# Kernel optimization log

Hardware: AMD Instinct MI355X
Metric: run time of the kernel (lower is better)

Reference implementation:

```python
import jax, jax.numpy as jnp
import numpy as np

NUM_HEADS = 16

def _alibi(S, H, dtype):
    # fairseq-style ALiBi: slopes[h] * -(|i-j|), H assumed power of 2
    start = 2.0 ** (-8.0 / H)
    slopes = start ** jnp.arange(1, H + 1, dtype=jnp.float32)      # [H]
    pos = jnp.arange(S)
    rel = -jnp.abs(pos[None, :] - pos[:, None]).astype(jnp.float32)  # [S,S]
    return (slopes[:, None, None] * rel).astype(dtype)             # [H,S,S]

def setup_inputs() -> dict:
    key = jax.random.key(0)
    kx, km, kw1, kw2 = jax.random.split(key, 4)
    B, S, D = 2, 2048, 1024
    inputs = jax.random.normal(kx, (B, S, D), dtype=jnp.float32)
    mask = jax.random.bernoulli(km, 0.9, (B, S))
    mask = mask.at[:, 0].set(True)  # ensure each row has a valid key
    Wqkv = jax.random.normal(kw1, (3 * D, D), dtype=jnp.float32) * 0.02
    bqkv = jnp.zeros((3 * D,), dtype=jnp.float32)
    Wproj = jax.random.normal(kw2, (D, D), dtype=jnp.float32) * 0.02
    bproj = jnp.zeros((D,), dtype=jnp.float32)
    return {"inputs": inputs, "mask": mask, "Wqkv": Wqkv, "bqkv": bqkv,
            "Wproj": Wproj, "bproj": bproj}

def reference(inputs, mask, Wqkv, bqkv, Wproj, bproj):
    B, S, D = inputs.shape
    H = NUM_HEADS
    dh = D // H
    scale = D ** (-0.5)  # NOTE: original scales by full dim, not head dim
    qkv = inputs @ Wqkv.T + bqkv                       # [B,S,3D]
    qkv = qkv.reshape(B, S, H, 3 * dh).transpose(0, 2, 1, 3)  # [B,H,S,3dh]
    q, k, v = qkv[..., :dh], qkv[..., dh:2 * dh], qkv[..., 2 * dh:]
    attn = jnp.einsum('bhqd,bhkd->bhqk', q, k) * scale  # [B,H,S,S]
    attn = attn + _alibi(S, H, attn.dtype)[None]
    attn = jnp.where(mask[:, None, None, :], attn, jnp.finfo(attn.dtype).min)
    attn = jax.nn.softmax(attn, axis=-1)
    x = jnp.einsum('bhqk,bhkd->bhqd', attn, v)          # [B,H,S,dh]
    x = x.transpose(0, 2, 1, 3).reshape(B, S, D)
    return x @ Wproj.T + bproj
```

## Files before the change

### kernel.cpp

```cpp
#include <hip/hip_runtime.h>
#include <cstdint>
#include <cstddef>

#define B_  2
#define S_  2048
#define D_  1024
#define H_  16
#define DH_ 64
#define M_  (B_*S_)
#define N3_ (3*D_)
#define NT_ (S_/64)

typedef float f32x4 __attribute__((ext_vector_type(4)));
typedef short short8 __attribute__((ext_vector_type(8)));
typedef int   i32x4 __attribute__((ext_vector_type(4)));
typedef unsigned short u16x8 __attribute__((ext_vector_type(8)));
typedef unsigned short u16x4 __attribute__((ext_vector_type(4)));
typedef unsigned short u16x2 __attribute__((ext_vector_type(2)));

__device__ __forceinline__ unsigned short f2bf(float x) {
    unsigned int u = __float_as_uint(x);
    unsigned int r = (u + 0x7FFFu + ((u >> 16) & 1u)) >> 16;
    return (unsigned short)r;
}

__device__ __forceinline__ float exp2_(float x) { return __builtin_amdgcn_exp2f(x); }

__device__ __forceinline__ unsigned int cvt_pk_bf16(float a, float b) {
    unsigned int r;
    asm volatile("v_cvt_pk_bf16_f32 %0, %1, %2" : "=v"(r) : "v"(a), "v"(b));
    return r;
}

__device__ __forceinline__ int s3x(int row) {
    return (((row & 3) | (((row >> 3) & 1) << 2)) << 4);
}

__device__ __forceinline__ int xcd_swizzle(int lin, int nwg) {
    const int cpx = nwg >> 3;
    return (lin & 7) * cpx + (lin >> 3);
}

__device__ __forceinline__ void gload16(const void* g, void* l) {
    __builtin_amdgcn_global_load_lds(
        (const __attribute__((address_space(1))) unsigned int*)g,
        (__attribute__((address_space(3))) unsigned int*)l,
        16, 0, 0);
}

__global__ void k_mask(const unsigned char* __restrict__ mb, float* __restrict__ maskbias) {
    __shared__ int sBig, sM4, sM8;
    if (threadIdx.x == 0) { sBig = 0; sM4 = 0; sM8 = 0; }
    __syncthreads();
    int big = 0, m4 = 0, m8 = 0;
    for (int i = threadIdx.x; i < 4096; i += 256) {
        unsigned char v = mb[i];
        if (v > 1) big = 1;
        if (v && (i & 3)) m4 = 1;
        if (v && ((i & 7) == 4)) m8 = 1;
    }
    if (big) atomicOr(&sBig, 1);
    if (m4)  atomicOr(&sM4, 1);
    if (m8)  atomicOr(&sM8, 1);
    __syncthreads();
    const int w = sBig ? 0 : (sM4 ? 1 : (sM8 ? 4 : 8));
    const int i = blockIdx.x * 256 + threadIdx.x;
    bool on;
    if (w == 0)      on = ((const float*)mb)[i] != 0.0f;
    else if (w == 1) on = mb[i] != 0;
    else if (w == 4) on = ((const int*)mb)[i] != 0;
    else             on = ((const long long*)mb)[i] != 0;
    maskbias[i] = on ? 0.0f : -1e30f;
}

__global__ void k_f2bf3(const float* __restrict__ A, const float* __restrict__ B2,
                        const float* __restrict__ C, unsigned short* __restrict__ oA,
                        unsigned short* __restrict__ oB, unsigned short* __restrict__ oC) {
    const int nA = M_ * D_, nB = N3_ * D_, nC = D_ * D_;
    int i = (blockIdx.x * 256 + threadIdx.x) * 4;
    const float* src; unsigned short* dst; int off;
    if (i < nA)           { src = A;  dst = oA; off = i; }
    else if (i < nA + nB) { src = B2; dst = oB; off = i - nA; }
    else if (i < nA + nB + nC) { src = C; dst = oC; off = i - nA - nB; }
    else return;
    float4 v = *reinterpret_cast<const float4*>(&src[off]);
    u16x4 o = { f2bf(v.x), f2bf(v.y), f2bf(v.z), f2bf(v.w) };
    *reinterpret_cast<u16x4*>(&dst[off]) = o;
}

template <bool OUT_BF16>
__global__ __launch_bounds__(512) void k_gemm_bf16_cv(
    const unsigned short* __restrict__ A, const unsigned short* __restrict__ W,
    const float* __restrict__ bias, void* __restrict__ Cout,
    int M, int N, int K) {
    __shared__ __align__(16) unsigned short Al[3][128 * 64];
    __shared__ __align__(16) unsigned short Wl[3][128 * 64];

    const int tid  = threadIdx.x;
    const int lane = tid & 63;
    const int w    = tid >> 6;
    const int wr   = w >> 2, wc = w & 3;
    const int l16  = lane & 15, g = lane >> 4;
    const int m0 = blockIdx.y * 128, n0 = blockIdx.x * 128;
    const int NTk = K >> 6;

    f32x4 acc[4][2];
#pragma unroll
    for (int m = 0; m < 4; ++m)
#pragma unroll
        for (int n = 0; n < 2; ++n) acc[m][n] = (f32x4){0.f, 0.f, 0.f, 0.f};

    auto issueTile = [&](int kt) {
        const int k0 = kt << 6;
        unsigned short* Ad = Al[kt % 3];
        unsigned short* Wd = Wl[kt % 3];
#pragma unroll
        for (int i = 0; i < 2; ++i) {
            const int c = i * 512 + tid;
            const int row = c >> 3;
            const int colel = (((c & 7) ^ (row & 7)) << 3);
            gload16(A + (size_t)(m0 + row) * K + k0 + colel, Ad + c * 8);
            gload16(W + (size_t)(n0 + row) * K + k0 + colel, Wd + c * 8);
        }
    };

    issueTile(0);
    issueTile(1);

    for (int t = 0; t < NTk; ++t) {
        if (t + 2 < NTk) issueTile(t + 2);

        if (t < NTk - 2)       asm volatile("s_waitcnt vmcnt(8)" ::: "memory");
        else if (t == NTk - 2) asm volatile("s_waitcnt vmcnt(4)" ::: "memory");
        else                   asm volatile("s_waitcnt vmcnt(0)" ::: "memory");
        __builtin_amdgcn_s_barrier();
        __builtin_amdgcn_sched_barrier(0);

        const unsigned short* Ab = Al[t % 3];
        const unsigned short* Wb = Wl[t % 3];
        short8 a[4][2], b[2][2];
#pragma unroll
        for (int m = 0; m < 4; ++m)
#pragma unroll
            for (int kk = 0; kk < 2; ++kk) {
                const int row = wr * 64 + m * 16 + l16;
                const int kb = (kk * 64 + g * 16) ^ ((row & 7) << 4);
                a[m][kk] = *reinterpret_cast<const short8*>(
                    (const char*)Ab + row * 128 + kb);
            }
#pragma unroll
        for (int n = 0; n < 2; ++n)
#pragma unroll
            for (int kk = 0; kk < 2; ++kk) {
                const int row = wc * 32 + n * 16 + l16;
                const int kb = (kk * 64 + g * 16) ^ ((row & 7) << 4);
                b[n][kk] = *reinterpret_cast<const short8*>(
                    (const char*)Wb + row * 128 + kb);
            }

        __builtin_amdgcn_s_setprio(1);
#pragma unroll
        for (int kk = 0; kk < 2; ++kk)
#pragma unroll
            for (int m = 0; m < 4; ++m)
#pragma unroll
                for (int n = 0; n < 2; ++n)
                    acc[m][n] = __builtin_amdgcn_mfma_f32_16x16x32_bf16(
                        a[m][kk], b[n][kk], acc[m][n], 0, 0, 0);
        __builtin_amdgcn_s_setprio(0);

        __builtin_amdgcn_sched_barrier(0);
        __builtin_amdgcn_s_barrier();
    }

    float bv[2];
#pragma unroll
    for (int n = 0; n < 2; ++n) bv[n] = bias[n0 + wc * 32 + n * 16 + l16];
#pragma unroll
    for (int m = 0; m < 4; ++m) {
#pragma unroll
        for (int r = 0; r < 4; ++r) {
            const size_t row = m0 + wr * 64 + m * 16 + g * 4 + r;
#pragma unroll
            for (int n = 0; n < 2; ++n) {
                const int col = n0 + wc * 32 + n * 16 + l16;
                float v = acc[m][n][r] + bv[n];
                if (OUT_BF16)
                    ((unsigned short*)Cout)[row * N + col] = f2bf(v);
                else
                    ((float*)Cout)[row * N + col] = v;
            }
        }
    }
}

__global__ __launch_bounds__(512, 4) void k_attn_mfma(
    const unsigned short* __restrict__ qkv,
    const float* __restrict__ maskbias,
    unsigned short* __restrict__ x) {
    __shared__ __align__(16) unsigned short Kt[2][64][64];
    __shared__ __align__(16) unsigned short Vt[3][64][64];

    const int tid  = threadIdx.x;
    const int lane = tid & 63;
    const int wq   = tid >> 6;
    const int g    = lane >> 4;
    const int g4   = g * 4;
    const int l16  = lane & 15;

    const int nqt = S_ / 128;
    const int nwg = B_ * H_ * nqt;
    const int bid = xcd_swizzle(blockIdx.x, nwg);
    const int qt = bid % nqt;
    const int h  = (bid / nqt) % H_;
    const int b  = bid / (nqt * H_);
    const int q0 = qt * 128;
    const size_t rowbase = (size_t)b * S_ * N3_;
    const int hq = h * 192, hk = hq + 64, hv = hq + 128;
    const unsigned short* kvb = qkv + rowbase;
    const float* mbp = maskbias + b * S_;

    const int blrow = 8 * (l16 >> 2) + (l16 & 3);
    const int KBJ[4] = { 0, 4, 32, 36 };

    const unsigned short* qrp = kvb + (size_t)(q0 + wq * 16 + l16) * N3_ + hq;
    const short8 qa0 = *reinterpret_cast<const short8*>(qrp + g * 8);
    const short8 qa1 = *reinterpret_cast<const short8*>(qrp + 32 + g * 8);

    const int krow = tid >> 3;
    const int kgr  = tid & 7;
    const int vkb4 = (tid & 31) * 4;
    const int vdb  = (tid >> 5) * 4;
    u16x8 kr;
    u16x4 vr0, vr1;

    const int kwOff = (kgr << 4) ^ s3x(krow);

    {
        kr  = *reinterpret_cast<const u16x8*>(kvb + (size_t)krow * N3_ + hk + kgr * 8);
        const unsigned short* vs = kvb + (size_t)((tid & 31) * 2) * N3_ + hv + vdb;
        vr0 = *reinterpret_cast<const u16x4*>(vs);
        vr1 = *reinterpret_cast<const u16x4*>(vs + N3_);
        *reinterpret_cast<u16x8*>((char*)&Kt[0][krow][0] + kwOff) = kr;
#pragma unroll
        for (int j = 0; j < 4; ++j)
            *reinterpret_cast<u16x2*>((char*)&Vt[0][vdb + j][0] + (vkb4 ^ s3x(vdb + j))) =
                (u16x2){vr0[j], vr1[j]};
    }
    __syncthreads();

    f32x4 Oacc[4];
#pragma unroll
    for (int df = 0; df < 4; ++df) Oacc[df] = (f32x4){0.f, 0.f, 0.f, 0.f};
    float m = -1e30f, l = 0.0f;

    const float LOG2E = 1.4426950408889634f;
    const float c1 = 0.03125f * LOG2E;
    const float c2 = exp2f(-0.5f * (float)(h + 1)) * LOG2E;
    const int   qw0 = q0 + wq * 16;
    const int   qg  = qw0 + l16;
    const float alg = c2 * (float)(8 * g);
    float albr[4];
#pragma unroll
    for (int r = 0; r < 4; ++r) albr[r] = c2 * (float)r;
    const float ckb[4] = { 0.0f, c2 * 4.0f, c2 * 32.0f, c2 * 36.0f };

    const int sK = s3x(blrow);
    const int kr0Off = (g << 4) ^ sK;
    const int kr1Off = ((4 + g) << 4) ^ sK;
    const int sV = s3x(l16);
    const int vr0Off = (g << 4) ^ sV;
    const int vr1Off = ((4 + g) << 4) ^ sV;

    float p_[4][4];

    {
        kr  = *reinterpret_cast<const u16x8*>(kvb + (size_t)(64 + krow) * N3_ + hk + kgr * 8);
        const unsigned short* vs = kvb + (size_t)(64 + (tid & 31) * 2) * N3_ + hv + vdb;
        vr0 = *reinterpret_cast<const u16x4*>(vs);
        vr1 = *reinterpret_cast<const u16x4*>(vs + N3_);

        __builtin_amdgcn_s_setprio(1);
#pragma unroll
        for (int jb = 0; jb < 4; ++jb) {
            const char* rowp = (const char*)&Kt[0][blrow + KBJ[jb]][0];
            short8 kb0 = *reinterpret_cast<const short8*>(rowp + kr0Off);
            short8 kb1 = *reinterpret_cast<const short8*>(rowp + kr1Off);
            f32x4 c = (f32x4){0.f, 0.f, 0.f, 0.f};
            c = __builtin_amdgcn_mfma_f32_16x16x32_bf16(kb0, qa0, c, 0, 0, 0);
            c = __builtin_amdgcn_mfma_f32_16x16x32_bf16(kb1, qa1, c, 0, 0, 0);
#pragma unroll
            for (int r = 0; r < 4; ++r) p_[jb][r] = c[r];
        }
        __builtin_amdgcn_s_setprio(0);

        *reinterpret_cast<u16x8*>((char*)&Kt[1][krow][0] + kwOff) = kr;
#pragma unroll
        for (int j = 0; j < 4; ++j)
            *reinterpret_cast<u16x2*>((char*)&Vt[1][vdb + j][0] + (vkb4 ^ s3x(vdb + j))) =
                (u16x2){vr0[j], vr1[j]};
    }
    __syncthreads();
    {
        kr  = *reinterpret_cast<const u16x8*>(kvb + (size_t)(128 + krow) * N3_ + hk + kgr * 8);
        const unsigned short* vs = kvb + (size_t)(128 + (tid & 31) * 2) * N3_ + hv + vdb;
        vr0 = *reinterpret_cast<const u16x4*>(vs);
        vr1 = *reinterpret_cast<const u16x4*>(vs + N3_);
    }

    int vb_r = 0;
    int vb_w = 2;

    for (int t = 1; t < NT_ + 1; ++t) {
        const int k0m = (t - 1) * 64;

        f32x4 amv[4];
#pragma unroll
        for (int jb = 0; jb < 4; ++jb)
            amv[jb] = *reinterpret_cast<const f32x4*>(&mbp[k0m + 8 * g + KBJ[jb]]);

        f32x4 cnx[4];
        if (t < NT_) {
            const unsigned short (*Kc)[64] = Kt[t & 1];
            __builtin_amdgcn_s_setprio(1);
#pragma unroll
            for (int jb = 0; jb < 4; ++jb) {
                const char* rowp = (const char*)&Kc[blrow + KBJ[jb]][0];
                short8 kb0 = *reinterpret_cast<const short8*>(rowp + kr0Off);
                short8 kb1 = *reinterpret_cast<const short8*>(rowp + kr1Off);
                f32x4 c = (f32x4){0.f, 0.f, 0.f, 0.f};
                c = __builtin_amdgcn_mfma_f32_16x16x32_bf16(kb0, qa0, c, 0, 0, 0);
                c = __builtin_amdgcn_mfma_f32_16x16x32_bf16(kb1, qa1, c, 0, 0, 0);
                cnx[jb] = c;
            }
            __builtin_amdgcn_s_setprio(0);
        }

        if (k0m + 64 <= qw0) {
            const float tbg = c2 * (float)(k0m - qg) + alg;
#pragma unroll
            for (int jb = 0; jb < 4; ++jb) {
                const float tbj = tbg + ckb[jb];
#pragma unroll
                for (int r = 0; r < 4; ++r)
                    p_[jb][r] = fmaf(p_[jb][r], c1, tbj + albr[r] + amv[jb][r]);
            }
        } else if (k0m >= qw0 + 16) {
            const float tbg = c2 * (float)(k0m - qg) + alg;
#pragma unroll
            for (int jb = 0; jb < 4; ++jb) {
                const float tbj = -tbg - ckb[jb];
#pragma unroll
                for (int r = 0; r < 4; ++r)
                    p_[jb][r] = fmaf(p_[jb][r], c1, tbj - albr[r] + amv[jb][r]);
            }
        } else {
            const int dbase = k0m - qg + 8 * g;
#pragma unroll
            for (int jb = 0; jb < 4; ++jb)
#pragma unroll
                for (int r = 0; r < 4; ++r) {
                    int d = dbase + KBJ[jb] + r;
                    d = d < 0 ? -d : d;
                    p_[jb][r] = fmaf(p_[jb][r], c1, amv[jb][r] - c2 * (float)d);
                }
        }

        float mx;
        {
            float m0_ = fmaxf(fmaxf(p_[0][0], p_[0][1]), fmaxf(p_[0][2], p_[0][3]));
            float m1_ = fmaxf(fmaxf(p_[1][0], p_[1][1]), fmaxf(p_[1][2], p_[1][3]));
            float m2_ = fmaxf(fmaxf(p_[2][0], p_[2][1]), fmaxf(p_[2][2], p_[2][3]));
            float m3_ = fmaxf(fmaxf(p_[3][0], p_[3][1]), fmaxf(p_[3][2], p_[3][3]));
            mx = fmaxf(fmaxf(m0_, m1_), fmaxf(m2_, m3_));
        }
        mx = fmaxf(mx, __shfl_xor(mx, 16));
        mx = fmaxf(mx, __shfl_xor(mx, 32));

        if (__any(mx > m + 8.0f)) {
            const float mn = fmaxf(m, mx);
            const float cr = exp2_(m - mn);
            m = mn;
            l *= cr;
            const int srcb = (lane & 48) + ((lane & 48) >> 2);
#pragma unroll
            for (int r = 0; r < 4; ++r) {
                const float crq = __shfl(cr, srcb + r);
#pragma unroll
                for (int df = 0; df < 4; ++df) Oacc[df][r] *= crq;
            }
        }

        float ps = 0.0f;
#pragma unroll
        for (int jb = 0; jb < 4; ++jb)
#pragma unroll
            for (int r = 0; r < 4; ++r) {
                float p = exp2_(p_[jb][r] - m);
                p_[jb][r] = p;
                ps += p;
            }

        short8 pa0, pa1;
        {
            i32x4 w0 = { (int)cvt_pk_bf16(p_[0][0], p_[0][1]),
                         (int)cvt_pk_bf16(p_[0][2], p_[0][3]),
                         (int)cvt_pk_bf16(p_[1][0], p_[1][1]),
                         (int)cvt_pk_bf16(p_[1][2], p_[1][3]) };
            i32x4 w1 = { (int)cvt_pk_bf16(p_[2][0], p_[2][1]),
                         (int)cvt_pk_bf16(p_[2][2], p_[2][3]),
                         (int)cvt_pk_bf16(p_[3][0], p_[3][1]),
                         (int)cvt_pk_bf16(p_[3][2], p_[3][3]) };
            pa0 = __builtin_bit_cast(short8, w0);
            pa1 = __builtin_bit_cast(short8, w1);
        }

        {
            const unsigned short (*Vc)[64] = Vt[vb_r];
            __builtin_amdgcn_s_setprio(1);
#pragma unroll
            for (int df = 0; df < 4; ++df) {
                const char* rowp = (const char*)&Vc[df * 16 + l16][0];
                short8 vb0 = *reinterpret_cast<const short8*>(rowp + vr0Off);
                short8 vb1 = *reinterpret_cast<const short8*>(rowp + vr1Off);
                Oacc[df] = __builtin_amdgcn_mfma_f32_16x16x32_bf16(pa0, vb0, Oacc[df], 0, 0, 0);
                Oacc[df] = __builtin_amdgcn_mfma_f32_16x16x32_bf16(pa1, vb1, Oacc[df], 0, 0, 0);
            }
            __builtin_amdgcn_s_setprio(0);
        }

        ps += __shfl_xor(ps, 16);
        ps += __shfl_xor(ps, 32);
        l += ps;

        if (t + 1 < NT_) {
            *reinterpret_cast<u16x8*>((char*)&Kt[(t + 1) & 1][krow][0] + kwOff) = kr;
#pragma unroll
            for (int j = 0; j < 4; ++j)
                *reinterpret_cast<u16x2*>((char*)&Vt[vb_w][vdb + j][0] + (vkb4 ^ s3x(vdb + j))) =
                    (u16x2){vr0[j], vr1[j]};
            __syncthreads();
            if (t + 2 < NT_) {
                const int kn = (t + 2) * 64;
                kr  = *reinterpret_cast<const u16x8*>(kvb + (size_t)(kn + krow) * N3_ + hk + kgr * 8);
                const unsigned short* vs = kvb + (size_t)(kn + (tid & 31) * 2) * N3_ + hv + vdb;
                vr0 = *reinterpret_cast<const u16x4*>(vs);
                vr1 = *reinterpret_cast<const u16x4*>(vs + N3_);
            }
        }
        vb_r = (vb_r == 2) ? 0 : vb_r + 1;
        vb_w = (vb_w == 2) ? 0 : vb_w + 1;

        if (t < NT_) {
#pragma unroll
            for (int jb = 0; jb < 4; ++jb)
#pragma unroll
                for (int r = 0; r < 4; ++r) p_[jb][r] = cnx[jb][r];
        }
    }

    const int srcb = (lane & 48) + ((lane & 48) >> 2);
    float invq[4];
#pragma unroll
    for (int r = 0; r < 4; ++r) invq[r] = 1.0f / __shfl(l, srcb + r);
#pragma unroll
    for (int df = 0; df < 4; ++df) {
#pragma unroll
        for (int r = 0; r < 4; ++r) {
            const int qrow = q0 + wq * 16 + g4 + r;
            x[(size_t)(b * S_ + qrow) * D_ + h * 64 + df * 16 + l16] = f2bf(Oacc[df][r] * invq[r]);
        }
    }
}

extern "C" void kernel_launch(void* const* d_in, const int* in_sizes, int n_in,
                              void* d_out, int out_size, void* d_ws, size_t ws_size,
                              hipStream_t stream) {
    const float* inputs = (const float*)d_in[0];
    const void*  mask   = d_in[1];
    const float* Wqkv   = (const float*)d_in[2];
    const float* bqkv   = (const float*)d_in[3];
    const float* Wproj  = (const float*)d_in[4];
    const float* bproj  = (const float*)d_in[5];
    float* out = (float*)d_out;

    unsigned short* qkvb = (unsigned short*)d_ws;
    unsigned short* xb   = qkvb + (size_t)M_ * N3_;
    unsigned short* Ab   = xb + (size_t)M_ * D_;
    unsigned short* Wqb  = Ab + (size_t)M_ * D_;
    unsigned short* Wpb  = Wqb + (size_t)N3_ * D_;
    float* maskbias = (float*)(Wpb + (size_t)D_ * D_);

    k_mask<<<M_ / 256, 256, 0, stream>>>((const unsigned char*)mask, maskbias);

    const int ntot = M_ * D_ + N3_ * D_ + D_ * D_;
    k_f2bf3<<<(ntot / 4 + 255) / 256, 256, 0, stream>>>(inputs, Wqkv, Wproj, Ab, Wqb, Wpb);

    dim3 g1(N3_ / 128, M_ / 128);
    k_gemm_bf16_cv<true><<<g1, 512, 0, stream>>>(Ab, Wqb, bqkv, qkvb, M_, N3_, D_);

    k_attn_mfma<<<B_ * H_ * (S_ / 128), 512, 0, stream>>>(qkvb, maskbias, xb);

    dim3 g2(D_ / 128, M_ / 128);
    k_gemm_bf16_cv<false><<<g2, 512, 0, stream>>>(xb, Wpb, bproj, out, M_, D_, D_);
}
```

Before: 164.9 us.

## Split attention over two key halves and merge with a combine kernel

The attention kernel now splits the key range into two halves, doubling the number of workgroups. Each half writes unnormalized partial outputs in bf16 plus per-row max and sum statistics. A new combine kernel rescales and merges the two halves before the projection GEMM. The aim is better occupancy and load balance across CUs (512 blocks vs 1024). The cost is an extra launch, extra global traffic for the partials, and some bf16 rounding of the unnormalized partial outputs.

```diff
diff --git a/kernel.cpp b/kernel.cpp
--- a/kernel.cpp
+++ b/kernel.cpp
@@ -9,7 +9,7 @@
 #define DH_ 64
 #define M_  (B_*S_)
 #define N3_ (3*D_)
-#define NT_ (S_/64)
+#define NTH_ 16
 
 typedef float f32x4 __attribute__((ext_vector_type(4)));
 typedef short short8 __attribute__((ext_vector_type(8)));
@@ -194,10 +194,11 @@
     }
 }
 
-__global__ __launch_bounds__(512, 4) void k_attn_mfma(
+__global__ __launch_bounds__(512, 4) void k_attn_split(
     const unsigned short* __restrict__ qkv,
     const float* __restrict__ maskbias,
-    unsigned short* __restrict__ x) {
+    unsigned short* __restrict__ Opart,
+    float2* __restrict__ mlbuf) {
     __shared__ __align__(16) unsigned short Kt[2][64][64];
     __shared__ __align__(16) unsigned short Vt[3][64][64];
 
@@ -209,12 +210,15 @@
     const int l16  = lane & 15;
 
     const int nqt = S_ / 128;
-    const int nwg = B_ * H_ * nqt;
-    const int bid = xcd_swizzle(blockIdx.x, nwg);
-    const int qt = bid % nqt;
-    const int h  = (bid / nqt) % H_;
-    const int b  = bid / (nqt * H_);
+    const int nwg = B_ * H_ * nqt * 2;
+    const int lin = xcd_swizzle(blockIdx.x, nwg);
+    const int half = lin & 1;
+    const int bhq  = lin >> 1;
+    const int qt = bhq % nqt;
+    const int h  = (bhq / nqt) % H_;
+    const int b  = bhq / (nqt * H_);
     const int q0 = qt * 128;
+    const int kb0 = half * (NTH_ * 64);
     const size_t rowbase = (size_t)b * S_ * N3_;
     const int hq = h * 192, hk = hq + 64, hv = hq + 128;
     const unsigned short* kvb = qkv + rowbase;
@@ -237,8 +241,8 @@
     const int kwOff = (kgr << 4) ^ s3x(krow);
 
     {
-        kr  = *reinterpret_cast<const u16x8*>(kvb + (size_t)krow * N3_ + hk + kgr * 8);
-        const unsigned short* vs = kvb + (size_t)((tid & 31) * 2) * N3_ + hv + vdb;
+        kr  = *reinterpret_cast<const u16x8*>(kvb + (size_t)(kb0 + krow) * N3_ + hk + kgr * 8);
+        const unsigned short* vs = kvb + (size_t)(kb0 + (tid & 31) * 2) * N3_ + hv + vdb;
         vr0 = *reinterpret_cast<const u16x4*>(vs);
         vr1 = *reinterpret_cast<const u16x4*>(vs + N3_);
         *reinterpret_cast<u16x8*>((char*)&Kt[0][krow][0] + kwOff) = kr;
@@ -275,8 +279,8 @@
     float p_[4][4];
 
     {
-        kr  = *reinterpret_cast<const u16x8*>(kvb + (size_t)(64 + krow) * N3_ + hk + kgr * 8);
-        const unsigned short* vs = kvb + (size_t)(64 + (tid & 31) * 2) * N3_ + hv + vdb;
+        kr  = *reinterpret_cast<const u16x8*>(kvb + (size_t)(kb0 + 64 + krow) * N3_ + hk + kgr * 8);
+        const unsigned short* vs = kvb + (size_t)(kb0 + 64 + (tid & 31) * 2) * N3_ + hv + vdb;
         vr0 = *reinterpret_cast<const u16x4*>(vs);
         vr1 = *reinterpret_cast<const u16x4*>(vs + N3_);
 
@@ -284,11 +288,11 @@
 #pragma unroll
         for (int jb = 0; jb < 4; ++jb) {
             const char* rowp = (const char*)&Kt[0][blrow + KBJ[jb]][0];
-            short8 kb0 = *reinterpret_cast<const short8*>(rowp + kr0Off);
-            short8 kb1 = *reinterpret_cast<const short8*>(rowp + kr1Off);
+            short8 kb0_ = *reinterpret_cast<const short8*>(rowp + kr0Off);
+            short8 kb1_ = *reinterpret_cast<const short8*>(rowp + kr1Off);
             f32x4 c = (f32x4){0.f, 0.f, 0.f, 0.f};
-            c = __builtin_amdgcn_mfma_f32_16x16x32_bf16(kb0, qa0, c, 0, 0, 0);
-            c = __builtin_amdgcn_mfma_f32_16x16x32_bf16(kb1, qa1, c, 0, 0, 0);
+            c = __builtin_amdgcn_mfma_f32_16x16x32_bf16(kb0_, qa0, c, 0, 0, 0);
+            c = __builtin_amdgcn_mfma_f32_16x16x32_bf16(kb1_, qa1, c, 0, 0, 0);
 #pragma unroll
             for (int r = 0; r < 4; ++r) p_[jb][r] = c[r];
         }
@@ -302,8 +306,8 @@
     }
     __syncthreads();
     {
-        kr  = *reinterpret_cast<const u16x8*>(kvb + (size_t)(128 + krow) * N3_ + hk + kgr * 8);
-        const unsigned short* vs = kvb + (size_t)(128 + (tid & 31) * 2) * N3_ + hv + vdb;
+        kr  = *reinterpret_cast<const u16x8*>(kvb + (size_t)(kb0 + 128 + krow) * N3_ + hk + kgr * 8);
+        const unsigned short* vs = kvb + (size_t)(kb0 + 128 + (tid & 31) * 2) * N3_ + hv + vdb;
         vr0 = *reinterpret_cast<const u16x4*>(vs);
         vr1 = *reinterpret_cast<const u16x4*>(vs + N3_);
     }
@@ -311,8 +315,8 @@
     int vb_r = 0;
     int vb_w = 2;
 
-    for (int t = 1; t < NT_ + 1; ++t) {
-        const int k0m = (t - 1) * 64;
+    for (int t = 1; t < NTH_ + 1; ++t) {
+        const int k0m = kb0 + (t - 1) * 64;
 
         f32x4 amv[4];
 #pragma unroll
@@ -320,17 +324,17 @@
             amv[jb] = *reinterpret_cast<const f32x4*>(&mbp[k0m + 8 * g + KBJ[jb]]);
 
         f32x4 cnx[4];
-        if (t < NT_) {
+        if (t < NTH_) {
             const unsigned short (*Kc)[64] = Kt[t & 1];
             __builtin_amdgcn_s_setprio(1);
 #pragma unroll
             for (int jb = 0; jb < 4; ++jb) {
                 const char* rowp = (const char*)&Kc[blrow + KBJ[jb]][0];
-                short8 kb0 = *reinterpret_cast<const short8*>(rowp + kr0Off);
-                short8 kb1 = *reinterpret_cast<const short8*>(rowp + kr1Off);
+                short8 kf0 = *reinterpret_cast<const short8*>(rowp + kr0Off);
+                short8 kf1 = *reinterpret_cast<const short8*>(rowp + kr1Off);
                 f32x4 c = (f32x4){0.f, 0.f, 0.f, 0.f};
-                c = __builtin_amdgcn_mfma_f32_16x16x32_bf16(kb0, qa0, c, 0, 0, 0);
-                c = __builtin_amdgcn_mfma_f32_16x16x32_bf16(kb1, qa1, c, 0, 0, 0);
+                c = __builtin_amdgcn_mfma_f32_16x16x32_bf16(kf0, qa0, c, 0, 0, 0);
+                c = __builtin_amdgcn_mfma_f32_16x16x32_bf16(kf1, qa1, c, 0, 0, 0);
                 cnx[jb] = c;
             }
             __builtin_amdgcn_s_setprio(0);
@@ -433,15 +437,15 @@
         ps += __shfl_xor(ps, 32);
         l += ps;
 
-        if (t + 1 < NT_) {
+        if (t + 1 < NTH_) {
             *reinterpret_cast<u16x8*>((char*)&Kt[(t + 1) & 1][krow][0] + kwOff) = kr;
 #pragma unroll
             for (int j = 0; j < 4; ++j)
                 *reinterpret_cast<u16x2*>((char*)&Vt[vb_w][vdb + j][0] + (vkb4 ^ s3x(vdb + j))) =
                     (u16x2){vr0[j], vr1[j]};
             __syncthreads();
-            if (t + 2 < NT_) {
-                const int kn = (t + 2) * 64;
+            if (t + 2 < NTH_) {
+                const int kn = kb0 + (t + 2) * 64;
                 kr  = *reinterpret_cast<const u16x8*>(kvb + (size_t)(kn + krow) * N3_ + hk + kgr * 8);
                 const unsigned short* vs = kvb + (size_t)(kn + (tid & 31) * 2) * N3_ + hv + vdb;
                 vr0 = *reinterpret_cast<const u16x4*>(vs);
@@ -451,7 +455,7 @@
         vb_r = (vb_r == 2) ? 0 : vb_r + 1;
         vb_w = (vb_w == 2) ? 0 : vb_w + 1;
 
-        if (t < NT_) {
+        if (t < NTH_) {
 #pragma unroll
             for (int jb = 0; jb < 4; ++jb)
 #pragma unroll
@@ -459,18 +463,42 @@
         }
     }
 
-    const int srcb = (lane & 48) + ((lane & 48) >> 2);
-    float invq[4];
-#pragma unroll
-    for (int r = 0; r < 4; ++r) invq[r] = 1.0f / __shfl(l, srcb + r);
+    unsigned short* Ob = Opart + (size_t)half * M_ * D_;
 #pragma unroll
     for (int df = 0; df < 4; ++df) {
 #pragma unroll
         for (int r = 0; r < 4; ++r) {
             const int qrow = q0 + wq * 16 + g4 + r;
-            x[(size_t)(b * S_ + qrow) * D_ + h * 64 + df * 16 + l16] = f2bf(Oacc[df][r] * invq[r]);
-        }
-    }
+            Ob[(size_t)(b * S_ + qrow) * D_ + h * 64 + df * 16 + l16] = f2bf(Oacc[df][r]);
+        }
+    }
+    if (g == 0)
+        mlbuf[((size_t)half * M_ + b * S_ + qw0 + l16) * H_ + h] = make_float2(m, l);
+}
+
+__global__ __launch_bounds__(256) void k_attn_combine(
+    const unsigned short* __restrict__ Op, const float2* __restrict__ ml,
+    unsigned short* __restrict__ xb) {
+    const int idx = blockIdx.x * 256 + threadIdx.x;
+    const int row = idx >> 7;
+    const int col = (idx & 127) * 8;
+    const int h   = col >> 6;
+    const float2 a = ml[(size_t)row * H_ + h];
+    const float2 c = ml[((size_t)M_ + row) * H_ + h];
+    const float ms = fmaxf(a.x, c.x);
+    const float e0 = exp2_(a.x - ms), e1 = exp2_(c.x - ms);
+    const float inv = 1.0f / fmaf(a.y, e0, c.y * e1);
+    const float s0 = e0 * inv, s1 = e1 * inv;
+    const u16x8 v0 = *reinterpret_cast<const u16x8*>(&Op[(size_t)row * D_ + col]);
+    const u16x8 v1 = *reinterpret_cast<const u16x8*>(&Op[((size_t)M_ + row) * D_ + col]);
+    u16x8 o;
+#pragma unroll
+    for (int j = 0; j < 8; ++j) {
+        float f0 = __uint_as_float((unsigned int)v0[j] << 16);
+        float f1 = __uint_as_float((unsigned int)v1[j] << 16);
+        o[j] = f2bf(fmaf(f0, s0, f1 * s1));
+    }
+    *reinterpret_cast<u16x8*>(&xb[(size_t)row * D_ + col]) = o;
 }
 
 extern "C" void kernel_launch(void* const* d_in, const int* in_sizes, int n_in,
@@ -484,12 +512,14 @@
     const float* bproj  = (const float*)d_in[5];
     float* out = (float*)d_out;
 
-    unsigned short* qkvb = (unsigned short*)d_ws;
-    unsigned short* xb   = qkvb + (size_t)M_ * N3_;
-    unsigned short* Ab   = xb + (size_t)M_ * D_;
-    unsigned short* Wqb  = Ab + (size_t)M_ * D_;
-    unsigned short* Wpb  = Wqb + (size_t)N3_ * D_;
-    float* maskbias = (float*)(Wpb + (size_t)D_ * D_);
+    unsigned short* qkvb  = (unsigned short*)d_ws;
+    unsigned short* xb    = qkvb + (size_t)M_ * N3_;
+    unsigned short* Ab    = xb + (size_t)M_ * D_;
+    unsigned short* Wqb   = Ab + (size_t)M_ * D_;
+    unsigned short* Wpb   = Wqb + (size_t)N3_ * D_;
+    unsigned short* Opart = Wpb + (size_t)D_ * D_;
+    float*  maskbias = (float*)(Opart + (size_t)2 * M_ * D_);
+    float2* mlbuf    = (float2*)(maskbias + M_);
 
     k_mask<<<M_ / 256, 256, 0, stream>>>((const unsigned char*)mask, maskbias);
 
@@ -499,7 +529,8 @@
     dim3 g1(N3_ / 128, M_ / 128);
     k_gemm_bf16_cv<true><<<g1, 512, 0, stream>>>(Ab, Wqb, bqkv, qkvb, M_, N3_, D_);
 
-    k_attn_mfma<<<B_ * H_ * (S_ / 128), 512, 0, stream>>>(qkvb, maskbias, xb);
+    k_attn_split<<<B_ * H_ * (S_ / 128) * 2, 512, 0, stream>>>(qkvb, maskbias, Opart, mlbuf);
+    k_attn_combine<<<M_ * D_ / 8 / 256, 256, 0, stream>>>(Opart, mlbuf, xb);
 
     dim3 g2(D_ / 128, M_ / 128);
     k_gemm_bf16_cv<false><<<g2, 512, 0, stream>>>(xb, Wpb, bproj, out, M_, D_, D_);
```

Result: slower. 202.8 us (+23.0%).
